# Kernel tuning notes

Hardware: AMD Instinct MI355X
Metric: run time of the kernel (lower is better)

## Reference

```python
import jax, jax.numpy as jnp
import numpy as np

N = 200000
IN_CH = 128
HIDDEN = [512, 512, 256]
NUM_TYPES = 10


def hetero_linear(x, types, W, b):
    # y[n] = x[n] @ W[types[n]] + b[types[n]]
    # Loop over the small fixed set of types (grouped GEMM as masked dense GEMMs).
    out = jnp.zeros((x.shape[0], W.shape[2]), dtype=x.dtype)
    for t in range(W.shape[0]):
        yt = x @ W[t] + b[t]
        out = out + jnp.where((types == t)[:, None], yt, jnp.zeros((), x.dtype))
    return out


def setup_inputs() -> dict:
    key = jax.random.key(0)
    ks = jax.random.split(key, 8)
    dims = [IN_CH] + HIDDEN
    inp = {
        "x": jax.random.normal(ks[0], (N, IN_CH), dtype=jnp.float32),
        "atom_types": jax.random.randint(ks[1], (N,), 0, NUM_TYPES, dtype=jnp.int32),
    }
    for i in range(3):
        fan_in = dims[i]
        scale = 1.0 / np.sqrt(fan_in)
        inp[f"W{i}"] = jax.random.normal(ks[2 + 2 * i], (NUM_TYPES, dims[i], dims[i + 1]), dtype=jnp.float32) * scale
        inp[f"b{i}"] = jax.random.normal(ks[3 + 2 * i], (NUM_TYPES, dims[i + 1]), dtype=jnp.float32) * scale
    return inp


def reference(x, atom_types, W0, b0, W1, b1, W2, b2):
    h = jax.nn.relu(hetero_linear(x, atom_types, W0, b0))
    h = jax.nn.relu(hetero_linear(h, atom_types, W1, b1))
    return hetero_linear(h, atom_types, W2, b2)
```

## Files before the change

### kernel.cpp

```cpp
#include <hip/hip_runtime.h>
#include <stdint.h>

typedef float  f32x4  __attribute__((ext_vector_type(4)));
typedef short  bf16x8 __attribute__((ext_vector_type(8)));

#define TYPES 10
#define D_IN  128
#define D_H1  512
#define D_H2  512
#define D_OUT 256

__device__ __forceinline__ unsigned short f2bf(float f) {
  union { float f; unsigned u; } v; v.f = f;
  unsigned u = v.u;
  return (unsigned short)((u + 0x7FFFu + ((u >> 16) & 1u)) >> 16);
}

__device__ __forceinline__ void async16(void* lds, const void* g) {
  __builtin_amdgcn_global_load_lds(
      (const __attribute__((address_space(1))) void*)g,
      (__attribute__((address_space(3))) void*)lds, 16, 0, 0);
}

__global__ void k_init(int* meta) {
  if (threadIdx.x < 48) meta[threadIdx.x] = 0;
}

__global__ void k_hist(const int* __restrict__ types, int n, int* __restrict__ meta) {
  __shared__ int lc[TYPES];
  if (threadIdx.x < TYPES) lc[threadIdx.x] = 0;
  __syncthreads();
  int i = blockIdx.x * 256 + threadIdx.x;
  if (i < n) atomicAdd(&lc[types[i]], 1);
  __syncthreads();
  if (threadIdx.x < TYPES && lc[threadIdx.x]) atomicAdd(&meta[threadIdx.x], lc[threadIdx.x]);
}

__global__ void k_scan(int* meta) {
  if (threadIdx.x == 0) {
    int off = 0;
    for (int t = 0; t < TYPES; ++t) {
      meta[16 + t] = off;
      off += ((meta[t] + 255) >> 8) << 8;
    }
    meta[26] = off;
  }
}

__global__ void k_scatter(const int* __restrict__ types, int n,
                          int* __restrict__ meta, int* __restrict__ perm) {
  __shared__ int lc[TYPES], lbase[TYPES];
  if (threadIdx.x < TYPES) lc[threadIdx.x] = 0;
  __syncthreads();
  int i = blockIdx.x * 256 + threadIdx.x;
  int t = 0, loc = 0;
  bool ok = i < n;
  if (ok) { t = types[i]; loc = atomicAdd(&lc[t], 1); }
  __syncthreads();
  if (threadIdx.x < TYPES) {
    int c = lc[threadIdx.x];
    lbase[threadIdx.x] = c ? atomicAdd(&meta[32 + threadIdx.x], c) : 0;
  }
  __syncthreads();
  if (ok) perm[meta[16 + t] + lbase[t] + loc] = i;
}

__global__ void k_gather(const float* __restrict__ x, const int* __restrict__ perm,
                         const int* __restrict__ meta, unsigned short* __restrict__ xs) {
  int p = blockIdx.x * 8 + (threadIdx.x >> 5);
  if (p >= meta[26]) return;
  int t = 0;
  while (p >= meta[17 + t]) t++;
  int e = (threadIdx.x & 31) * 4;
  unsigned short o0, o1, o2, o3;
  if (p - meta[16 + t] < meta[t]) {
    const float4 v = *(const float4*)(x + (size_t)perm[p] * D_IN + e);
    o0 = f2bf(v.x); o1 = f2bf(v.y); o2 = f2bf(v.z); o3 = f2bf(v.w);
  } else {
    o0 = o1 = o2 = o3 = 0;
  }
  *(ushort4*)(xs + (size_t)p * D_IN + e) = make_ushort4(o0, o1, o2, o3);
}

__global__ void k_wtrans_all(const float* __restrict__ W0a, const float* __restrict__ W1a,
                             const float* __restrict__ W2a,
                             unsigned short* __restrict__ wt0, unsigned short* __restrict__ wt1,
                             unsigned short* __restrict__ wt2) {
  int b = blockIdx.x;
  const float* W; unsigned short* Wt; int K, NOUT, t, local;
  if (b < 160)      { W = W0a; Wt = wt0; K = 128; NOUT = 512; t = b / 16; local = b % 16; }
  else if (b < 800) { b -= 160; W = W1a; Wt = wt1; K = 512; NOUT = 512; t = b / 64; local = b % 64; }
  else              { b -= 800; W = W2a; Wt = wt2; K = 512; NOUT = 256; t = b / 32; local = b % 32; }
  int ntn = NOUT >> 6;
  int kb = local / ntn, nb = local % ntn;
  __shared__ unsigned short tile[64][65];
  const float* src = W + (size_t)t * K * NOUT + (size_t)(kb * 64) * NOUT + nb * 64;
  int c = threadIdx.x & 63;
  int r0 = threadIdx.x >> 6;
  #pragma unroll
  for (int i = 0; i < 16; ++i) {
    int r = r0 * 16 + i;
    tile[r][c] = f2bf(src[(size_t)r * NOUT + c]);
  }
  __syncthreads();
  unsigned short* dst = Wt + (size_t)t * NOUT * K + (size_t)(nb * 64) * K + kb * 64;
  #pragma unroll
  for (int i = 0; i < 16; ++i) {
    int nn = r0 * 16 + i;
    dst[(size_t)nn * K + c] = tile[c][nn];
  }
}

template <int K, int NOUT, bool RELU, bool FINAL>
__launch_bounds__(512, 2)
__global__ void k_gemm(const unsigned short* __restrict__ A,
                       const unsigned short* __restrict__ Wt,
                       const float* __restrict__ bias,
                       unsigned short* __restrict__ H,
                       float* __restrict__ OUT,
                       const int* __restrict__ meta,
                       const int* __restrict__ perm) {
  constexpr int nKT = K / 64;
  __shared__ char lds[131072];

  int NXB = gridDim.x;
  int nwg = NXB * (int)gridDim.y;
  int raw = blockIdx.x + blockIdx.y * NXB;
  int q = nwg >> 3, rr = nwg & 7;
  int xcd = raw & 7, idx = raw >> 3;
  int swz = (xcd < rr ? xcd * (q + 1) : rr * (q + 1) + (xcd - rr) * q) + idx;
  int bx = swz % NXB, by = swz / NXB;

  int row0 = by * 256;
  if (row0 >= meta[26]) return;
  int t = 0;
  while (row0 >= meta[17 + t]) t++;
  int seg = meta[16 + t], cnt = meta[t];
  int tid = threadIdx.x, lane = tid & 63, wid = tid >> 6;
  int wr = (wid >> 2) * 128, wc = (wid & 3) * 64;
  int ah = wid >> 2, bh = (wid & 3) >> 1, clb = (wid & 1) * 64;
  int col0 = bx * 256;
  const char* Ag = (const char*)(A + (size_t)row0 * K);
  const char* Bg = (const char*)(Wt + ((size_t)t * NOUT + col0) * K);

  int gsrc = ((tid & 7) ^ ((tid >> 3) & 7)) * 16;
  const char* aS = Ag + (size_t)(tid >> 3) * (2 * K) + gsrc;
  const char* bS = Bg + (size_t)(tid >> 3) * (2 * K) + gsrc;

  auto stage = [&](int kt, int sub) {
    if (kt >= nKT) return;
    int h = sub & 1, du = kt & 1;
    char* dst = lds + ((sub < 2) ? 0 : 65536) + (du * 2 + h) * 16384 + wid * 1024;
    const char* base = (sub < 2) ? aS : bS;
    const char* src = base + (size_t)(h * 128) * (2 * K) + (size_t)kt * 128;
    async16(dst,        src);
    async16(dst + 8192, src + (size_t)64 * (2 * K));
  };

  f32x4 acc[8][4] = {};
  int rA = lane & 15, qoff = (lane >> 4) * 16, xr = (lane & 7) << 4;

  stage(0, 0); stage(0, 1); stage(0, 2); stage(0, 3); stage(1, 0);
  asm volatile("s_waitcnt vmcnt(2)" ::: "memory");
  __builtin_amdgcn_s_barrier();

  for (int g = 0; g < nKT; ++g) {
    int d = g & 1;
    const char* Au = lds + (d * 2 + ah) * 16384;
    const char* Bu = lds + 65536 + (d * 2 + bh) * 16384;
    bf16x8 a[4], b0[4], b1[4];

    #pragma unroll
    for (int m = 0; m < 4; ++m) {
      int lr = m * 16 + rA;
      a[m] = *(const bf16x8*)(Au + lr * 128 + (qoff ^ xr));
    }
    #pragma unroll
    for (int n = 0; n < 4; ++n) {
      int cl = clb + n * 16 + rA;
      b0[n] = *(const bf16x8*)(Bu + cl * 128 + (qoff ^ xr));
      b1[n] = *(const bf16x8*)(Bu + cl * 128 + ((64 + qoff) ^ xr));
    }
    stage(g + 1, 1);
    asm volatile("s_waitcnt lgkmcnt(8)" ::: "memory");
    __builtin_amdgcn_s_barrier();
    asm volatile("s_waitcnt lgkmcnt(0)" ::: "memory");
    __builtin_amdgcn_s_setprio(1);
    #pragma unroll
    for (int m = 0; m < 4; ++m)
      #pragma unroll
      for (int n = 0; n < 4; ++n)
        acc[m][n] = __builtin_amdgcn_mfma_f32_16x16x32_bf16(a[m], b0[n], acc[m][n], 0, 0, 0);
    __builtin_amdgcn_s_setprio(0);
    __builtin_amdgcn_s_barrier();

    #pragma unroll
    for (int m = 0; m < 4; ++m) {
      int lr = m * 16 + rA;
      a[m] = *(const bf16x8*)(Au + lr * 128 + ((64 + qoff) ^ xr));
    }
    stage(g + 1, 2);
    __builtin_amdgcn_s_barrier();
    asm volatile("s_waitcnt lgkmcnt(0)" ::: "memory");
    __builtin_amdgcn_s_setprio(1);
    #pragma unroll
    for (int m = 0; m < 4; ++m)
      #pragma unroll
      for (int n = 0; n < 4; ++n)
        acc[m][n] = __builtin_amdgcn_mfma_f32_16x16x32_bf16(a[m], b1[n], acc[m][n], 0, 0, 0);
    __builtin_amdgcn_s_setprio(0);
    __builtin_amdgcn_s_barrier();

    #pragma unroll
    for (int m = 0; m < 4; ++m) {
      int lr = 64 + m * 16 + rA;
      a[m] = *(const bf16x8*)(Au + lr * 128 + (qoff ^ xr));
    }
    stage(g + 1, 3);
    __builtin_amdgcn_s_barrier();
    asm volatile("s_waitcnt lgkmcnt(0)" ::: "memory");
    __builtin_amdgcn_s_setprio(1);
    #pragma unroll
    for (int m = 0; m < 4; ++m)
      #pragma unroll
      for (int n = 0; n < 4; ++n)
        acc[4 + m][n] = __builtin_amdgcn_mfma_f32_16x16x32_bf16(a[m], b0[n], acc[4 + m][n], 0, 0, 0);
    __builtin_amdgcn_s_setprio(0);
    __builtin_amdgcn_s_barrier();

    #pragma unroll
    for (int m = 0; m < 4; ++m) {
      int lr = 64 + m * 16 + rA;
      a[m] = *(const bf16x8*)(Au + lr * 128 + ((64 + qoff) ^ xr));
    }
    stage(g + 2, 0);
    __builtin_amdgcn_s_barrier();
    asm volatile("s_waitcnt lgkmcnt(0)" ::: "memory");
    __builtin_amdgcn_s_setprio(1);
    #pragma unroll
    for (int m = 0; m < 4; ++m)
      #pragma unroll
      for (int n = 0; n < 4; ++n)
        acc[4 + m][n] = __builtin_amdgcn_mfma_f32_16x16x32_bf16(a[m], b1[n], acc[4 + m][n], 0, 0, 0);
    __builtin_amdgcn_s_setprio(0);
    if (g + 1 < nKT) {
      if (g + 2 < nKT) asm volatile("s_waitcnt vmcnt(2)" ::: "memory");
      else             asm volatile("s_waitcnt vmcnt(0)" ::: "memory");
    }
    __builtin_amdgcn_s_barrier();
  }

  int cA = lane & 15, rE = (lane >> 4) * 4;
  float bv[4];
  #pragma unroll
  for (int ni = 0; ni < 4; ++ni) bv[ni] = bias[t * NOUT + col0 + wc + ni * 16 + cA];
  char* cb = (char*)lds;

  if (!FINAL) {
    #pragma unroll
    for (int mi = 0; mi < 8; ++mi) {
      int rowoff = (mi >> 2) * 64 + (mi & 3) * 16;
      #pragma unroll
      for (int e = 0; e < 4; ++e) {
        int row = wr + rowoff + rE + e;
        int sw = (row & 7) << 4;
        #pragma unroll
        for (int ni = 0; ni < 4; ++ni) {
          float v = acc[mi][ni][e] + bv[ni];
          if (RELU) v = fmaxf(v, 0.f);
          int col = wc + ni * 16 + cA;
          *(unsigned short*)(cb + ((row * 512 + col * 2) ^ sw)) = f2bf(v);
        }
      }
    }
    __builtin_amdgcn_s_barrier();
    #pragma unroll 4
    for (int r = 0; r < 16; ++r) {
      int row = wid * 32 + r * 2 + (lane >> 5);
      int addr = row * 512 + ((((lane & 31) * 16)) ^ ((row & 7) << 4));
      bf16x8 v = *(const bf16x8*)(cb + addr);
      *(bf16x8*)(H + (size_t)(row0 + row) * NOUT + col0 + (lane & 31) * 8) = v;
    }
  } else {
    int myhalf = (wid & 3) >> 1;
    #pragma unroll
    for (int p = 0; p < 2; ++p) {
      if (myhalf == p) {
        int colh = wc & 127;
        #pragma unroll
        for (int mi = 0; mi < 8; ++mi) {
          int rowoff = (mi >> 2) * 64 + (mi & 3) * 16;
          #pragma unroll
          for (int e = 0; e < 4; ++e) {
            int row = wr + rowoff + rE + e;
            int sw = (row & 7) << 4;
            #pragma unroll
            for (int ni = 0; ni < 4; ++ni) {
              float v = acc[mi][ni][e] + bv[ni];
              if (RELU) v = fmaxf(v, 0.f);
              int col = colh + ni * 16 + cA;
              *(float*)(cb + ((row * 512 + col * 4) ^ sw)) = v;
            }
          }
        }
      }
      __builtin_amdgcn_s_barrier();
      #pragma unroll 4
      for (int r = 0; r < 16; ++r) {
        int row = wid * 32 + r * 2 + (lane >> 5);
        int gr = row0 + row;
        int addr = row * 512 + ((((lane & 31) * 16)) ^ ((row & 7) << 4));
        float4 v = *(const float4*)(cb + addr);
        if (gr - seg < cnt) {
          int pr = perm[gr];
          *(float4*)(OUT + (size_t)pr * NOUT + p * (NOUT / 2) + (lane & 31) * 4) = v;
        }
      }
      if (p == 0) __builtin_amdgcn_s_barrier();
    }
  }
}

extern "C" void kernel_launch(void* const* d_in, const int* in_sizes, int n_in,
                              void* d_out, int out_size, void* d_ws, size_t ws_size,
                              hipStream_t stream) {
  const float* x     = (const float*)d_in[0];
  const int*   types = (const int*)d_in[1];
  const float* W0    = (const float*)d_in[2];
  const float* b0    = (const float*)d_in[3];
  const float* W1    = (const float*)d_in[4];
  const float* b1    = (const float*)d_in[5];
  const float* W2    = (const float*)d_in[6];
  const float* b2    = (const float*)d_in[7];
  float* out = (float*)d_out;
  int n = in_sizes[1];
  int RB = (n + 255) / 256 + TYPES;
  size_t NPAD = (size_t)RB * 256;

  char* ws = (char*)d_ws;
  int* meta = (int*)ws;
  int* perm = (int*)(ws + 1024);
  size_t off = 1024 + NPAD * 4;
  off = (off + 255) & ~(size_t)255;
  unsigned short* wt0 = (unsigned short*)(ws + off); off += (size_t)TYPES * D_H1 * D_IN * 2;
  unsigned short* wt1 = (unsigned short*)(ws + off); off += (size_t)TYPES * D_H2 * D_H1 * 2;
  unsigned short* wt2 = (unsigned short*)(ws + off); off += (size_t)TYPES * D_OUT * D_H2 * 2;
  off = (off + 255) & ~(size_t)255;
  unsigned short* B1 = (unsigned short*)(ws + off); off += NPAD * 512 * 2;
  unsigned short* B2 = (unsigned short*)(ws + off); off += NPAD * 512 * 2;

  int hb = (n + 255) / 256;
  k_init<<<1, 64, 0, stream>>>(meta);
  k_hist<<<hb, 256, 0, stream>>>(types, n, meta);
  k_scan<<<1, 64, 0, stream>>>(meta);
  k_scatter<<<hb, 256, 0, stream>>>(types, n, meta, perm);
  k_gather<<<RB * 32, 256, 0, stream>>>(x, perm, meta, B1);
  k_wtrans_all<<<1120, 256, 0, stream>>>(W0, W1, W2, wt0, wt1, wt2);

  k_gemm<D_IN, D_H1, true,  false><<<dim3(D_H1 / 256, RB), 512, 0, stream>>>(B1, wt0, b0, B2, nullptr, meta, perm);
  k_gemm<D_H1, D_H2, true,  false><<<dim3(D_H2 / 256, RB), 512, 0, stream>>>(B2, wt1, b1, B1, nullptr, meta, perm);
  k_gemm<D_H2, D_OUT, false, true ><<<dim3(D_OUT / 256, RB), 512, 0, stream>>>(B1, wt2, b2, nullptr, out, meta, perm);
}
```

Measured before the change: 425.2 us.

## Fuse row gather and bf16 conversion into first-layer GEMM

```diff
diff --git a/kernel.cpp b/kernel.cpp
--- a/kernel.cpp
+++ b/kernel.cpp
@@ -63,23 +63,6 @@
   }
   __syncthreads();
   if (ok) perm[meta[16 + t] + lbase[t] + loc] = i;
-}
-
-__global__ void k_gather(const float* __restrict__ x, const int* __restrict__ perm,
-                         const int* __restrict__ meta, unsigned short* __restrict__ xs) {
-  int p = blockIdx.x * 8 + (threadIdx.x >> 5);
-  if (p >= meta[26]) return;
-  int t = 0;
-  while (p >= meta[17 + t]) t++;
-  int e = (threadIdx.x & 31) * 4;
-  unsigned short o0, o1, o2, o3;
-  if (p - meta[16 + t] < meta[t]) {
-    const float4 v = *(const float4*)(x + (size_t)perm[p] * D_IN + e);
-    o0 = f2bf(v.x); o1 = f2bf(v.y); o2 = f2bf(v.z); o3 = f2bf(v.w);
-  } else {
-    o0 = o1 = o2 = o3 = 0;
-  }
-  *(ushort4*)(xs + (size_t)p * D_IN + e) = make_ushort4(o0, o1, o2, o3);
 }
 
 __global__ void k_wtrans_all(const float* __restrict__ W0a, const float* __restrict__ W1a,
@@ -108,6 +91,141 @@
   for (int i = 0; i < 16; ++i) {
     int nn = r0 * 16 + i;
     dst[(size_t)nn * K + c] = tile[c][nn];
+  }
+}
+
+__launch_bounds__(512, 2)
+__global__ void k_gemm1(const float* __restrict__ x,
+                        const unsigned short* __restrict__ Wt,
+                        const float* __restrict__ bias,
+                        unsigned short* __restrict__ H,
+                        const int* __restrict__ meta,
+                        const int* __restrict__ perm) {
+  constexpr int K = 128, NOUT = 512;
+  __shared__ char lds[131072];
+
+  int NXB = gridDim.x;
+  int nwg = NXB * (int)gridDim.y;
+  int raw = blockIdx.x + blockIdx.y * NXB;
+  int q = nwg >> 3, rr = nwg & 7;
+  int xcd = raw & 7, idx = raw >> 3;
+  int swz = (xcd < rr ? xcd * (q + 1) : rr * (q + 1) + (xcd - rr) * q) + idx;
+  int bx = swz % NXB, by = swz / NXB;
+
+  int row0 = by * 256;
+  if (row0 >= meta[26]) return;
+  int t = 0;
+  while (row0 >= meta[17 + t]) t++;
+  int seg = meta[16 + t], cnt = meta[t];
+  int tid = threadIdx.x, lane = tid & 63, wid = tid >> 6;
+  int wr = (wid >> 2) * 128, wc = (wid & 3) * 64;
+  int ah = wid >> 2, bh = (wid & 3) >> 1;
+  int col0 = bx * 256;
+  const char* Bg = (const char*)(Wt + ((size_t)t * NOUT + col0) * K);
+
+  int gl = tid & 7, lrb = tid >> 3;
+  int gsrc = (gl ^ (lrb & 7)) * 16;
+  const char* bS = Bg + (size_t)lrb * (2 * K) + gsrc;
+
+  #pragma unroll
+  for (int h = 0; h < 2; ++h)
+    #pragma unroll
+    for (int kt = 0; kt < 2; ++kt) {
+      char* dst = lds + 65536 + (h * 2 + kt) * 16384 + wid * 1024;
+      const char* src = bS + (size_t)(h * 128) * (2 * K) + kt * 128;
+      async16(dst,        src);
+      async16(dst + 8192, src + (size_t)64 * (2 * K));
+    }
+
+  #pragma unroll
+  for (int h = 0; h < 2; ++h)
+    #pragma unroll
+    for (int i = 0; i < 2; ++i) {
+      int lr = i * 64 + lrb;
+      int p = row0 + h * 128 + lr;
+      bool ok = (unsigned)(p - seg) < (unsigned)cnt;
+      int sr = ok ? perm[p] : 0;
+      int ksw = (gl ^ (lr & 7)) * 8;
+      #pragma unroll
+      for (int kt = 0; kt < 2; ++kt) {
+        bf16x8 v;
+        if (ok) {
+          const float* sp = x + (size_t)sr * K + kt * 64 + ksw;
+          float4 f0 = *(const float4*)(sp);
+          float4 f1 = *(const float4*)(sp + 4);
+          v[0] = (short)f2bf(f0.x); v[1] = (short)f2bf(f0.y);
+          v[2] = (short)f2bf(f0.z); v[3] = (short)f2bf(f0.w);
+          v[4] = (short)f2bf(f1.x); v[5] = (short)f2bf(f1.y);
+          v[6] = (short)f2bf(f1.z); v[7] = (short)f2bf(f1.w);
+        } else {
+          v = bf16x8{0, 0, 0, 0, 0, 0, 0, 0};
+        }
+        *(bf16x8*)(lds + (h * 2 + kt) * 16384 + lr * 128 + gl * 16) = v;
+      }
+    }
+
+  __syncthreads();
+
+  f32x4 acc[8][4] = {};
+  int rA = lane & 15, qoff = (lane >> 4) * 16, xr = (lane & 7) << 4;
+  #pragma unroll
+  for (int kt = 0; kt < 2; ++kt) {
+    const char* Au = lds + (ah * 2 + kt) * 16384;
+    const char* Bu = lds + 65536 + (bh * 2 + kt) * 16384;
+    bf16x8 b0[4], b1[4];
+    #pragma unroll
+    for (int n = 0; n < 4; ++n) {
+      int cl = (wid & 1) * 64 + n * 16 + rA;
+      b0[n] = *(const bf16x8*)(Bu + cl * 128 + (qoff ^ xr));
+      b1[n] = *(const bf16x8*)(Bu + cl * 128 + ((64 + qoff) ^ xr));
+    }
+    #pragma unroll
+    for (int mh = 0; mh < 2; ++mh) {
+      bf16x8 a0[4], a1[4];
+      #pragma unroll
+      for (int m = 0; m < 4; ++m) {
+        int lr = mh * 64 + m * 16 + rA;
+        a0[m] = *(const bf16x8*)(Au + lr * 128 + (qoff ^ xr));
+        a1[m] = *(const bf16x8*)(Au + lr * 128 + ((64 + qoff) ^ xr));
+      }
+      #pragma unroll
+      for (int m = 0; m < 4; ++m)
+        #pragma unroll
+        for (int n = 0; n < 4; ++n) {
+          acc[mh * 4 + m][n] = __builtin_amdgcn_mfma_f32_16x16x32_bf16(a0[m], b0[n], acc[mh * 4 + m][n], 0, 0, 0);
+          acc[mh * 4 + m][n] = __builtin_amdgcn_mfma_f32_16x16x32_bf16(a1[m], b1[n], acc[mh * 4 + m][n], 0, 0, 0);
+        }
+    }
+  }
+  __builtin_amdgcn_s_barrier();
+
+  int cA = lane & 15, rE = (lane >> 4) * 4;
+  float bv[4];
+  #pragma unroll
+  for (int ni = 0; ni < 4; ++ni) bv[ni] = bias[t * NOUT + col0 + wc + ni * 16 + cA];
+  char* cb = (char*)lds;
+  #pragma unroll
+  for (int mi = 0; mi < 8; ++mi) {
+    int rowoff = (mi >> 2) * 64 + (mi & 3) * 16;
+    #pragma unroll
+    for (int e = 0; e < 4; ++e) {
+      int row = wr + rowoff + rE + e;
+      int sw = (row & 7) << 4;
+      #pragma unroll
+      for (int ni = 0; ni < 4; ++ni) {
+        float v = fmaxf(acc[mi][ni][e] + bv[ni], 0.f);
+        int col = wc + ni * 16 + cA;
+        *(unsigned short*)(cb + ((row * 512 + col * 2) ^ sw)) = f2bf(v);
+      }
+    }
+  }
+  __builtin_amdgcn_s_barrier();
+  #pragma unroll 4
+  for (int r = 0; r < 16; ++r) {
+    int row = wid * 32 + r * 2 + (lane >> 5);
+    int addr = row * 512 + ((((lane & 31) * 16)) ^ ((row & 7) << 4));
+    bf16x8 v = *(const bf16x8*)(cb + addr);
+    *(bf16x8*)(H + (size_t)(row0 + row) * NOUT + col0 + (lane & 31) * 8) = v;
   }
 }
 
@@ -354,10 +472,9 @@
   k_hist<<<hb, 256, 0, stream>>>(types, n, meta);
   k_scan<<<1, 64, 0, stream>>>(meta);
   k_scatter<<<hb, 256, 0, stream>>>(types, n, meta, perm);
-  k_gather<<<RB * 32, 256, 0, stream>>>(x, perm, meta, B1);
   k_wtrans_all<<<1120, 256, 0, stream>>>(W0, W1, W2, wt0, wt1, wt2);
 
-  k_gemm<D_IN, D_H1, true,  false><<<dim3(D_H1 / 256, RB), 512, 0, stream>>>(B1, wt0, b0, B2, nullptr, meta, perm);
+  k_gemm1<<<dim3(D_H1 / 256, RB), 512, 0, stream>>>(x, wt0, b0, B2, meta, perm);
   k_gemm<D_H1, D_H2, true,  false><<<dim3(D_H2 / 256, RB), 512, 0, stream>>>(B2, wt1, b1, B1, nullptr, meta, perm);
   k_gemm<D_H2, D_OUT, false, true ><<<dim3(D_OUT / 256, RB), 512, 0, stream>>>(B1, wt2, b2, nullptr, out, meta, perm);
 }
```

Result: no change. 428.5 us (+0.8%).

## Add register-prefetched B-operand GEMM kernel for the middle layer

Applied to the files above, without the earlier changes.

```diff
diff --git a/kernel.cpp b/kernel.cpp
--- a/kernel.cpp
+++ b/kernel.cpp
@@ -108,6 +108,122 @@
   for (int i = 0; i < 16; ++i) {
     int nn = r0 * 16 + i;
     dst[(size_t)nn * K + c] = tile[c][nn];
+  }
+}
+
+__launch_bounds__(512, 2)
+__global__ void k_gemmR(const unsigned short* __restrict__ A,
+                        const unsigned short* __restrict__ Wt,
+                        const float* __restrict__ bias,
+                        unsigned short* __restrict__ H,
+                        const int* __restrict__ meta) {
+  constexpr int K = 512, NOUT = 512, nKT = 8, K2 = K * 2;
+  __shared__ char lds[131072];
+
+  int NXB = gridDim.x;
+  int nwg = NXB * (int)gridDim.y;
+  int raw = blockIdx.x + blockIdx.y * NXB;
+  int q = nwg >> 3, rr = nwg & 7;
+  int xcd = raw & 7, idx = raw >> 3;
+  int swz = (xcd < rr ? xcd * (q + 1) : rr * (q + 1) + (xcd - rr) * q) + idx;
+  int bx = swz % NXB, by = swz / NXB;
+
+  int row0 = by * 256;
+  if (row0 >= meta[26]) return;
+  int t = 0;
+  while (row0 >= meta[17 + t]) t++;
+  int tid = threadIdx.x, lane = tid & 63, wid = tid >> 6;
+  int mrow = (wid >> 1) * 64;
+  int ncg  = wid & 1;
+  int col0 = bx * 256;
+  const char* Ag = (const char*)(A + (size_t)row0 * K);
+  const char* Bg = (const char*)(Wt + ((size_t)t * NOUT + col0) * K);
+
+  int gsrc = ((tid & 7) ^ ((tid >> 3) & 7)) * 16;
+  const char* aS = Ag + (size_t)(tid >> 3) * K2 + gsrc;
+  auto stageA = [&](int kt) {
+    if (kt >= nKT) return;
+    char* dst = lds + (kt % 3) * 32768 + wid * 1024;
+    const char* src = aS + (size_t)kt * 128;
+    #pragma unroll
+    for (int i = 0; i < 4; ++i)
+      async16(dst + i * 8192, src + (size_t)(i * 64) * K2);
+  };
+
+  const char* bP = Bg + (size_t)(ncg * 128 + (lane & 15)) * K2 + (lane >> 4) * 16;
+  bf16x8 bA[8][2], bB[8][2];
+  auto loadB = [&](bf16x8 (&bb)[8][2], int kt) {
+    if (kt >= nKT) return;
+    #pragma unroll
+    for (int n = 0; n < 8; ++n)
+      #pragma unroll
+      for (int kk = 0; kk < 2; ++kk)
+        bb[n][kk] = *(const bf16x8*)(bP + (size_t)n * 16 * K2 + kt * 128 + kk * 64);
+  };
+
+  f32x4 acc[4][8] = {};
+  int rA = lane & 15, qk = (lane >> 4) * 16;
+  bf16x8 a[4][2];
+
+  loadB(bA, 0); stageA(0); stageA(1);
+  asm volatile("s_waitcnt vmcnt(0)" ::: "memory");
+  __builtin_amdgcn_s_barrier();
+
+  auto tile = [&](int g, bf16x8 (&bcur)[8][2], bf16x8 (&bnext)[8][2]) {
+    __builtin_amdgcn_sched_barrier(0);
+    const char* As = lds + (g % 3) * 32768;
+    #pragma unroll
+    for (int m = 0; m < 4; ++m) {
+      int R = mrow + m * 16 + rA;
+      #pragma unroll
+      for (int kk = 0; kk < 2; ++kk)
+        a[m][kk] = *(const bf16x8*)(As + R * 128 + ((kk * 64 + qk) ^ ((R & 7) << 4)));
+    }
+    loadB(bnext, g + 1);
+    stageA(g + 2);
+    __builtin_amdgcn_s_setprio(1);
+    #pragma unroll
+    for (int kk = 0; kk < 2; ++kk)
+      #pragma unroll
+      for (int m = 0; m < 4; ++m)
+        #pragma unroll
+        for (int n = 0; n < 8; ++n)
+          acc[m][n] = __builtin_amdgcn_mfma_f32_16x16x32_bf16(
+              a[m][kk], bcur[n][kk], acc[m][n], 0, 0, 0);
+    __builtin_amdgcn_s_setprio(0);
+    if (g + 2 < nKT)      asm volatile("s_waitcnt vmcnt(20)" ::: "memory");
+    else if (g + 1 < nKT) asm volatile("s_waitcnt vmcnt(16)" ::: "memory");
+    else                  asm volatile("s_waitcnt vmcnt(0)" ::: "memory");
+    __builtin_amdgcn_s_barrier();
+  };
+  #pragma unroll
+  for (int j = 0; j < nKT / 2; ++j) { tile(2 * j, bA, bB); tile(2 * j + 1, bB, bA); }
+
+  int cA = lane & 15, rE = (lane >> 4) * 4;
+  char* cb = (char*)lds;
+  float bv[8];
+  #pragma unroll
+  for (int n = 0; n < 8; ++n) bv[n] = bias[t * NOUT + col0 + ncg * 128 + n * 16 + cA];
+  #pragma unroll
+  for (int m = 0; m < 4; ++m)
+    #pragma unroll
+    for (int e = 0; e < 4; ++e) {
+      int row = mrow + m * 16 + rE + e;
+      int sw = (row & 7) << 4;
+      #pragma unroll
+      for (int n = 0; n < 8; ++n) {
+        float v = fmaxf(acc[m][n][e] + bv[n], 0.f);
+        int col = ncg * 128 + n * 16 + cA;
+        *(unsigned short*)(cb + ((row * 512 + col * 2) ^ sw)) = f2bf(v);
+      }
+    }
+  __builtin_amdgcn_s_barrier();
+  #pragma unroll 4
+  for (int r = 0; r < 16; ++r) {
+    int row = wid * 32 + r * 2 + (lane >> 5);
+    int addr = row * 512 + (((lane & 31) * 16) ^ ((row & 7) << 4));
+    bf16x8 v = *(const bf16x8*)(cb + addr);
+    *(bf16x8*)(H + (size_t)(row0 + row) * NOUT + col0 + (lane & 31) * 8) = v;
   }
 }
 
@@ -358,6 +474,6 @@
   k_wtrans_all<<<1120, 256, 0, stream>>>(W0, W1, W2, wt0, wt1, wt2);
 
   k_gemm<D_IN, D_H1, true,  false><<<dim3(D_H1 / 256, RB), 512, 0, stream>>>(B1, wt0, b0, B2, nullptr, meta, perm);
-  k_gemm<D_H1, D_H2, true,  false><<<dim3(D_H2 / 256, RB), 512, 0, stream>>>(B2, wt1, b1, B1, nullptr, meta, perm);
+  k_gemmR<<<dim3(D_H2 / 256, RB), 512, 0, stream>>>(B2, wt1, b1, B1, meta);
   k_gemm<D_H2, D_OUT, false, true ><<<dim3(D_OUT / 256, RB), 512, 0, stream>>>(B1, wt2, b2, nullptr, out, meta, perm);
 }
```

Result: slower. 868.2 us (+104.2%).
